# Performance work log

Hardware: AMD Instinct MI355X
Metric: run time of the kernel (lower is better)

Reference implementation:

```python
import jax, jax.numpy as jnp
import numpy as np

B, S, V = 2, 336, 8      # batch, seq_len, n_vars
D, H, P = 256, 8, 96     # d_model, num_heads, pred_len
DK = D // H
OUT_CHN = 8
EPS = 1e-5


def _layernorm(x, g, b):
    mu = jnp.mean(x, axis=-1, keepdims=True)
    var = jnp.var(x, axis=-1, keepdims=True)
    return (x - mu) * jax.lax.rsqrt(var + EPS) * g + b


def _attn_ff(src, Wq, bq, Wk, bk, Wv, bv, Wo, bo, ln1_g, ln1_b):
    # src: [N, L, D]; manual MHA + residual + layernorm (dropout=0)
    N, L, _ = src.shape
    q = (src @ Wq + bq).reshape(N, L, H, DK).transpose(0, 2, 1, 3)
    k = (src @ Wk + bk).reshape(N, L, H, DK).transpose(0, 2, 1, 3)
    v = (src @ Wv + bv).reshape(N, L, H, DK).transpose(0, 2, 1, 3)
    scores = jnp.einsum('nhqd,nhkd->nhqk', q, k) / np.sqrt(DK).astype(np.float32)
    attn = jax.nn.softmax(scores, axis=-1)
    o = jnp.einsum('nhqk,nhkd->nhqd', attn, v)
    o = o.transpose(0, 2, 1, 3).reshape(N, L, D) @ Wo + bo
    return _layernorm(src + o, ln1_g, ln1_b)


def setup_inputs() -> dict:
    key = jax.random.key(0)
    ks = jax.random.split(key, 8)
    s = 1.0 / np.sqrt(D)
    return {
        'x': jax.random.normal(ks[0], (B, S, V), dtype=jnp.float32),
        'emb_w': jax.random.normal(ks[1], (1, D), dtype=jnp.float32),
        'emb_b': jnp.zeros((D,), jnp.float32),
        'Wq': jax.random.normal(ks[2], (D, D), dtype=jnp.float32) * s,
        'bq': jnp.zeros((D,), jnp.float32),
        'Wk': jax.random.normal(ks[3], (D, D), dtype=jnp.float32) * s,
        'bk': jnp.zeros((D,), jnp.float32),
        'Wv': jax.random.normal(ks[4], (D, D), dtype=jnp.float32) * s,
        'bv': jnp.zeros((D,), jnp.float32),
        'Wo': jax.random.normal(ks[5], (D, D), dtype=jnp.float32) * s,
        'bo': jnp.zeros((D,), jnp.float32),
        'ln1_g': jnp.ones((D,), jnp.float32),
        'ln1_b': jnp.zeros((D,), jnp.float32),
        'norm_g': jnp.ones((D,), jnp.float32),
        'norm_b': jnp.zeros((D,), jnp.float32),
        'proj_w': jax.random.normal(ks[6], (S * D, P), dtype=jnp.float32) / np.sqrt(S * D).astype(np.float32),
        'proj_b': jnp.zeros((P,), jnp.float32),
    }


def reference(x, emb_w, emb_b, Wq, bq, Wk, bk, Wv, bv, Wo, bo,
              ln1_g, ln1_b, norm_g, norm_b, proj_w, proj_b):
    attn_p = (Wq, bq, Wk, bk, Wv, bv, Wo, bo, ln1_g, ln1_b)
    # x: [B,S,V] -> [B,V,S] -> embed each scalar to D
    e = x.transpose(0, 2, 1)[..., None] @ emb_w + emb_b  # [B,V,S,D]
    for _ in range(10):
        # attention over time axis (shared weights)
        e = _attn_ff(e.reshape(B * V, S, D), *attn_p).reshape(B, V, S, D)
        e = _layernorm(e.transpose(0, 2, 1, 3), norm_g, norm_b)  # [B,S,V,D]
        # attention over variable axis (same weights)
        e = _attn_ff(e.reshape(B * S, V, D), *attn_p).reshape(B, S, V, D)
        e = e.transpose(0, 2, 1, 3)  # [B,V,S,D]
    out = e.reshape(B, V, S * D) @ proj_w + proj_b  # [B,V,P]
    return out.transpose(0, 2, 1)[:, :, :OUT_CHN]  # [B,P,out_chn]
```

## Files before the change

### kernel.cpp

```cpp
#include <hip/hip_runtime.h>

#define SS 336
#define VV 8
#define DD 256
#define DKK 32
#define NTOK 5376
#define NTD (NTOK * DD)
#define ATT_SCALE 0.17677669529663687f
#define LN_EPS 1e-5f

typedef _Float16 f16x8 __attribute__((ext_vector_type(8)));
typedef _Float16 f16x4v __attribute__((ext_vector_type(4)));
typedef __attribute__((ext_vector_type(4))) float f32x4;

__device__ inline _Float16 f2h(float f) { return (_Float16)f; }

__global__ __launch_bounds__(256) void k_init(
    const float* __restrict__ Wq, const float* __restrict__ Wk,
    const float* __restrict__ Wv, const float* __restrict__ Wo,
    const float* __restrict__ x, const float* __restrict__ ew,
    const float* __restrict__ eb,
    _Float16* __restrict__ WT2, float* __restrict__ E,
    _Float16* __restrict__ E16, double* __restrict__ out64,
    int* __restrict__ cnt) {
  int bid = blockIdx.x;
  int tid = threadIdx.x;
  if (bid < 1024) {
    int z = bid >> 8;
    const float* W = (z == 0) ? Wq : (z == 1) ? Wk : (z == 2) ? Wv : Wo;
    int o = (bid & 255) * 256 + tid;
    int blk = o >> 9;
    int idx = o & 511;
    int lane = idx >> 3, j = idx & 7;
    int nt = blk >> 3, kb = blk & 7;
    int lcol = lane & 15, quad = lane >> 4;
    int n = nt * 16 + lcol;
    int k = kb * 32 + quad * 8 + j;
    WT2[(size_t)z * 65536 + o] = f2h(W[k * 256 + n]);
    if (bid == 0) {
      for (int i = tid; i < 1536; i += 256) atomicExch(&out64[i], 0.0);
      if (tid == 0) atomicExch(cnt, 0);
    }
  } else {
    int token = bid - 1024;
    int n = token / SS, s = token - n * SS;
    int b = n >> 3, v = n & 7;
    float xv = x[(b * SS + s) * VV + v];
    int d = tid;
    float val = fmaf(xv, ew[d], eb[d]);
    E[token * DD + d] = val;
    E16[token * DD + d] = f2h(val);
  }
}

#define KSTR 36
#define VTSTR 344
#define PSTR 72
#define QSTR 40
__global__ __launch_bounds__(512) void k_attn_time(
    const _Float16* __restrict__ Et16, const _Float16* __restrict__ Q16,
    const _Float16* __restrict__ K16, const _Float16* __restrict__ V16,
    const _Float16* __restrict__ WT2,
    const float* __restrict__ bq, const float* __restrict__ bk,
    const float* __restrict__ bv, _Float16* __restrict__ O16, int mode) {
  int qg = blockIdx.x, h = blockIdx.y, n = blockIdx.z;
  int tid = threadIdx.x;
  int wave = tid >> 6, lane = tid & 63;
  int quad = lane >> 4, lcol = lane & 15;

  __shared__ __align__(16) char SMRAW[143264];
  _Float16* Ks  = (_Float16*)SMRAW;
  _Float16* Vt  = (_Float16*)(SMRAW + 24192);
  _Float16* Qs  = (_Float16*)(SMRAW + 46240);
  _Float16* Wl  = (_Float16*)(SMRAW + 60320);
  _Float16* Ach = (_Float16*)(SMRAW + 109472);
  _Float16* PsB = (_Float16*)(mode ? SMRAW + 60320 : SMRAW + 46240);

  const size_t ebase = (size_t)(n * SS) * DD;
  const size_t base  = ebase + h * DKK;
  int qt0 = qg ? 11 : 0;
  int qtend = qg ? 21 : 11;

  const f32x4 z4 = {0.f, 0.f, 0.f, 0.f};

  if (mode) {
    {
      int h2 = h * 2;
      for (int c = tid; c < 3072; c += 512) {
        int ot = c >> 9, rest = c & 511;
        int z = (ot < 2) ? 1 : (ot < 4) ? 2 : 0;
        int nt = h2 + (ot & 1);
        *(f16x8*)&Wl[(ot << 12) + rest * 8] =
            *(const f16x8*)&WT2[(size_t)z * 65536 + nt * 4096 + rest * 8];
      }
      for (int c = tid; c < 272; c += 512) {
        if (c < 256) {
          int d = c >> 3, col = 336 + (c & 7);
          Vt[d * VTSTR + col] = (_Float16)0.f;
        } else {
          Vt[32 * VTSTR + (c - 256)] = (_Float16)0.f;
        }
      }
    }
    for (int ck = 0; ck < 6; ++ck) {
      int m0c = ck * 64;
      int nmt = (ck < 5) ? 4 : 1;
      __syncthreads();
      for (int c = tid; c < nmt * 16 * 32; c += 512) {
        int row = c >> 5, seg = c & 31;
        *(f16x8*)&Ach[row * 264 + seg * 8] =
            *(const f16x8*)&Et16[ebase + (size_t)(m0c + row) * 256 + seg * 8];
      }
      __syncthreads();
      int nU = nmt * 6;
      for (int u = wave; u < nU; u += 8) {
        int mtl = u / 6, ot = u % 6;
        int gt = ck * 4 + mtl;
        if (ot >= 4 && (gt < qt0 || gt >= qtend)) continue;
        f32x4 acc = z4;
#pragma unroll
        for (int kb = 0; kb < 8; ++kb) {
          f16x8 af = *(const f16x8*)&Ach[(mtl * 16 + lcol) * 264 + kb * 32 + quad * 8];
          f16x8 wf = *(const f16x8*)&Wl[(ot << 12) + kb * 512 + lane * 8];
          acc = __builtin_amdgcn_mfma_f32_16x16x32_f16(af, wf, acc, 0, 0, 0);
        }
        int dlo = ((ot & 1) << 4) + lcol;
        const float* bz = (ot < 2) ? bk : (ot < 4) ? bv : bq;
        float bval = bz[h * 32 + dlo];
        if (ot < 2) {
#pragma unroll
          for (int i = 0; i < 4; ++i)
            Ks[(m0c + mtl * 16 + quad * 4 + i) * KSTR + dlo] = f2h(acc[i] + bval);
        } else if (ot < 4) {
#pragma unroll
          for (int i = 0; i < 4; ++i)
            Vt[dlo * VTSTR + (m0c + mtl * 16 + quad * 4 + i)] = f2h(acc[i] + bval);
        } else {
          int ql = gt - qt0;
#pragma unroll
          for (int i = 0; i < 4; ++i)
            Qs[(ql * 16 + quad * 4 + i) * QSTR + dlo] = f2h(acc[i] + bval);
        }
      }
    }
    __syncthreads();
  } else {
    for (int c = tid; c < 1344; c += 512) {
      int row = c >> 2, part = c & 3;
      f16x8 kv = *(const f16x8*)&K16[base + (size_t)row * DD + part * 8];
      f16x4v klo = __builtin_shufflevector(kv, kv, 0, 1, 2, 3);
      f16x4v khi = __builtin_shufflevector(kv, kv, 4, 5, 6, 7);
      *(f16x4v*)&Ks[row * KSTR + part * 8] = klo;
      *(f16x4v*)&Ks[row * KSTR + part * 8 + 4] = khi;
      f16x8 vv = *(const f16x8*)&V16[base + (size_t)row * DD + part * 8];
#pragma unroll
      for (int j = 0; j < 8; ++j) Vt[(part * 8 + j) * VTSTR + row] = vv[j];
    }
    for (int c = tid; c < 272; c += 512) {
      if (c < 256) {
        int d = c >> 3, col = 336 + (c & 7);
        Vt[d * VTSTR + col] = (_Float16)0.f;
      } else {
        Vt[32 * VTSTR + (c - 256)] = (_Float16)0.f;
      }
    }
    __syncthreads();
  }

  _Float16* P = PsB + wave * (16 * PSTR);
  const f16x8 onesv = {(_Float16)1.f, (_Float16)1.f, (_Float16)1.f, (_Float16)1.f,
                       (_Float16)1.f, (_Float16)1.f, (_Float16)1.f, (_Float16)1.f};

  for (int qtile = qt0 + wave; qtile < qtend; qtile += 8) {
    int qb = qtile * 16;
    int ql = qtile - qt0;

    f16x8 qf;
    if (mode)
      qf = *(const f16x8*)&Qs[(ql * 16 + lcol) * QSTR + quad * 8];
    else
      qf = *(const f16x8*)&Q16[base + (size_t)(qb + lcol) * DD + quad * 8];
    f32x4 accA = {0.f, 0.f, 0.f, 0.f};
    f32x4 accB = {0.f, 0.f, 0.f, 0.f};
    f32x4 lacc = {0.f, 0.f, 0.f, 0.f};
    float m_[4] = {-1e30f, -1e30f, -1e30f, -1e30f};

    for (int T = 0; T < 6; ++T) {
      int k0 = T * 64;
      bool full = (T < 5);
      f32x4 s[4];
      {
        const _Float16* kp = &Ks[(k0 + lcol) * KSTR + quad * 8];
        f16x4v a0 = *(const f16x4v*)kp;
        f16x4v b0 = *(const f16x4v*)(kp + 4);
        f16x8 kf = __builtin_shufflevector(a0, b0, 0, 1, 2, 3, 4, 5, 6, 7);
        s[0] = __builtin_amdgcn_mfma_f32_16x16x32_f16(qf, kf, z4, 0, 0, 0);
      }
      if (full) {
#pragma unroll
        for (int u = 1; u < 4; ++u) {
          const _Float16* kp = &Ks[(k0 + u * 16 + lcol) * KSTR + quad * 8];
          f16x4v a0 = *(const f16x4v*)kp;
          f16x4v b0 = *(const f16x4v*)(kp + 4);
          f16x8 kf = __builtin_shufflevector(a0, b0, 0, 1, 2, 3, 4, 5, 6, 7);
          s[u] = __builtin_amdgcn_mfma_f32_16x16x32_f16(qf, kf, z4, 0, 0, 0);
        }
      } else {
        s[1] = z4; s[2] = z4; s[3] = z4;
      }
      float sc[4][4], p[4][4], corr[4];
#pragma unroll
      for (int u = 0; u < 4; ++u)
#pragma unroll
        for (int i = 0; i < 4; ++i)
          sc[u][i] = (u == 0 || full) ? s[u][i] * ATT_SCALE : -1e30f;
#pragma unroll
      for (int i = 0; i < 4; ++i) {
        float t2 = fmaxf(fmaxf(sc[0][i], sc[1][i]), fmaxf(sc[2][i], sc[3][i]));
        t2 = fmaxf(t2, __shfl_xor(t2, 1));
        t2 = fmaxf(t2, __shfl_xor(t2, 2));
        t2 = fmaxf(t2, __shfl_xor(t2, 4));
        t2 = fmaxf(t2, __shfl_xor(t2, 8));
        float nm = fmaxf(m_[i], t2);
        corr[i] = __expf(m_[i] - nm);
        m_[i] = nm;
#pragma unroll
        for (int u = 0; u < 4; ++u) p[u][i] = __expf(sc[u][i] - nm);
        accA[i] *= corr[i];
        accB[i] *= corr[i];
        lacc[i] *= corr[i];
      }
#pragma unroll
      for (int i = 0; i < 4; ++i)
#pragma unroll
        for (int u = 0; u < 4; ++u)
          P[(quad * 4 + i) * PSTR + u * 16 + lcol] = f2h(p[u][i]);
      f16x8 pf0 = *(const f16x8*)&P[lcol * PSTR + quad * 8];
      lacc = __builtin_amdgcn_mfma_f32_16x16x32_f16(pf0, onesv, lacc, 0, 0, 0);
      f16x8 va0 = *(const f16x8*)&Vt[lcol * VTSTR + k0 + quad * 8];
      f16x8 vb0 = *(const f16x8*)&Vt[(16 + lcol) * VTSTR + k0 + quad * 8];
      accA = __builtin_amdgcn_mfma_f32_16x16x32_f16(pf0, va0, accA, 0, 0, 0);
      accB = __builtin_amdgcn_mfma_f32_16x16x32_f16(pf0, vb0, accB, 0, 0, 0);
      if (full) {
        f16x8 pf1 = *(const f16x8*)&P[lcol * PSTR + 32 + quad * 8];
        lacc = __builtin_amdgcn_mfma_f32_16x16x32_f16(pf1, onesv, lacc, 0, 0, 0);
        f16x8 va1 = *(const f16x8*)&Vt[lcol * VTSTR + k0 + 32 + quad * 8];
        f16x8 vb1 = *(const f16x8*)&Vt[(16 + lcol) * VTSTR + k0 + 32 + quad * 8];
        accA = __builtin_amdgcn_mfma_f32_16x16x32_f16(pf1, va1, accA, 0, 0, 0);
        accB = __builtin_amdgcn_mfma_f32_16x16x32_f16(pf1, vb1, accB, 0, 0, 0);
      }
    }

#pragma unroll
    for (int i = 0; i < 4; ++i) {
      float inv = 1.f / lacc[i];
      P[(quad * 4 + i) * PSTR + lcol] = f2h(accA[i] * inv);
      P[(quad * 4 + i) * PSTR + 16 + lcol] = f2h(accB[i] * inv);
    }
    int row = lane >> 2, seg = lane & 3;
    f16x8 ov = *(const f16x8*)&P[row * PSTR + seg * 8];
    *(f16x8*)&O16[base + (size_t)(qb + row) * DD + seg * 8] = ov;
  }
}

__global__ __launch_bounds__(512) void k_mega_var(
    const _Float16* __restrict__ AO16, const _Float16* __restrict__ WT2,
    const float* __restrict__ bq, const float* __restrict__ bk,
    const float* __restrict__ bv, const float* __restrict__ bo,
    const float* __restrict__ g1, const float* __restrict__ c1,
    const float* __restrict__ gn, const float* __restrict__ bn,
    float* __restrict__ Etime, _Float16* __restrict__ Q16,
    _Float16* __restrict__ K16, _Float16* __restrict__ V16, int doqkv) {
  int tid = threadIdx.x;
  int wave = tid >> 6, lane = tid & 63;
  int quad = lane >> 4, lcol = lane & 15;

  __shared__ int rmapS[32];
  __shared__ _Float16 Af[32 * 264];
  __shared__ float Cf[32 * 260];
  __shared__ _Float16 QKVs[32 * 776];

  if (tid < 32) {
    int r2 = blockIdx.x * 32 + tid;
    int n_idx = r2 >> 3, v = r2 & 7;
    int b = n_idx / SS, s = n_idx - b * SS;
    rmapS[tid] = (b * VV + v) * SS + s;
  }
  __syncthreads();

  {
    int row = tid >> 4, seg = tid & 15;
    const _Float16* src = AO16 + (size_t)rmapS[row] * DD + seg * 16;
    _Float16* dst = Af + row * 264 + seg * 16;
    *(f16x8*)(dst) = *(const f16x8*)(src);
    *(f16x8*)(dst + 8) = *(const f16x8*)(src + 8);
  }
  __syncthreads();

  const _Float16* WoF = WT2 + (size_t)3 * 65536;

  {
    f32x4 acc[2][2] = {};
    for (int kb = 0; kb < 8; ++kb) {
      int k0 = kb * 32;
      f16x8 af0 = *(const f16x8*)&Af[lcol * 264 + k0 + quad * 8];
      f16x8 af1 = *(const f16x8*)&Af[(16 + lcol) * 264 + k0 + quad * 8];
#pragma unroll
      for (int nt = 0; nt < 2; ++nt) {
        f16x8 bfr = *(const f16x8*)&WoF[((wave * 2 + nt) * 8 + kb) * 512 + lane * 8];
        acc[0][nt] = __builtin_amdgcn_mfma_f32_16x16x32_f16(af0, bfr, acc[0][nt], 0, 0, 0);
        acc[1][nt] = __builtin_amdgcn_mfma_f32_16x16x32_f16(af1, bfr, acc[1][nt], 0, 0, 0);
      }
    }
#pragma unroll
    for (int mt = 0; mt < 2; ++mt) {
#pragma unroll
      for (int i = 0; i < 4; ++i) {
        int row = mt * 16 + quad * 4 + i;
        size_t rb = (size_t)rmapS[row] * 256;
#pragma unroll
        for (int nt = 0; nt < 2; ++nt) {
          int col = (wave * 2 + nt) * 16 + lcol;
          Cf[row * 260 + col] = acc[mt][nt][i] + bo[col] + Etime[rb + col];
        }
      }
    }
  }
  __syncthreads();

  {
    int row = tid >> 4, c0 = (tid & 15) * 16;
    float v[16];
#pragma unroll
    for (int j = 0; j < 16; ++j) v[j] = Cf[row * 260 + c0 + j];
#pragma unroll
    for (int pass = 0; pass < 2; ++pass) {
      const float* gg = pass ? gn : g1;
      const float* bb = pass ? bn : c1;
      float s = 0.f, q = 0.f;
#pragma unroll
      for (int j = 0; j < 16; ++j) { s += v[j]; q = fmaf(v[j], v[j], q); }
      s += __shfl_xor(s, 1); q += __shfl_xor(q, 1);
      s += __shfl_xor(s, 2); q += __shfl_xor(q, 2);
      s += __shfl_xor(s, 4); q += __shfl_xor(q, 4);
      s += __shfl_xor(s, 8); q += __shfl_xor(q, 8);
      float mu = s * (1.0f / 256.0f);
      float rs = rsqrtf(q * (1.0f / 256.0f) - mu * mu + LN_EPS);
#pragma unroll
      for (int j = 0; j < 16; ++j)
        v[j] = fmaf((v[j] - mu) * rs, gg[c0 + j], bb[c0 + j]);
    }
#pragma unroll
    for (int j = 0; j < 16; ++j) Cf[row * 260 + c0 + j] = v[j];
#pragma unroll
    for (int j8 = 0; j8 < 2; ++j8) {
      f16x8 h;
#pragma unroll
      for (int jj = 0; jj < 8; ++jj) h[jj] = f2h(v[j8 * 8 + jj]);
      *(f16x8*)&Af[row * 264 + c0 + j8 * 8] = h;
    }
  }
  __syncthreads();

  {
    f32x4 acc[2][6] = {};
    for (int kb = 0; kb < 8; ++kb) {
      int k0 = kb * 32;
      f16x8 af0 = *(const f16x8*)&Af[lcol * 264 + k0 + quad * 8];
      f16x8 af1 = *(const f16x8*)&Af[(16 + lcol) * 264 + k0 + quad * 8];
#pragma unroll
      for (int j = 0; j < 6; ++j) {
        int ntg = wave * 6 + j;
        f16x8 bfr = *(const f16x8*)&WT2[(size_t)(ntg * 8 + kb) * 512 + lane * 8];
        acc[0][j] = __builtin_amdgcn_mfma_f32_16x16x32_f16(af0, bfr, acc[0][j], 0, 0, 0);
        acc[1][j] = __builtin_amdgcn_mfma_f32_16x16x32_f16(af1, bfr, acc[1][j], 0, 0, 0);
      }
    }
#pragma unroll
    for (int j = 0; j < 6; ++j) {
      int ntg = wave * 6 + j;
      int colb = ntg * 16;
      int z = colb >> 8, coln = (colb & 255) + lcol;
      const float* bz = (z == 0) ? bq : (z == 1) ? bk : bv;
      float bval = bz[coln];
#pragma unroll
      for (int mt = 0; mt < 2; ++mt) {
#pragma unroll
        for (int i = 0; i < 4; ++i)
          QKVs[(mt * 16 + quad * 4 + i) * 776 + colb + lcol] = f2h(acc[mt][j][i] + bval);
      }
    }
  }
  __syncthreads();

  {
    int half = tid & 1, qi = (tid >> 1) & 7, h = (tid >> 4) & 7, ng = tid >> 7;
    int d0 = h * 32 + half * 16;
    const _Float16* Qp = &QKVs[(ng * 8 + qi) * 776 + d0];
    float qv[16];
#pragma unroll
    for (int j8 = 0; j8 < 2; ++j8) {
      f16x8 t = *(const f16x8*)(Qp + j8 * 8);
#pragma unroll
      for (int jj = 0; jj < 8; ++jj) qv[j8 * 8 + jj] = (float)t[jj];
    }
    float sc[8];
#pragma unroll
    for (int k = 0; k < 8; ++k) {
      const _Float16* Kp = &QKVs[(ng * 8 + k) * 776 + 256 + d0];
      float s = 0.f;
#pragma unroll
      for (int j8 = 0; j8 < 2; ++j8) {
        f16x8 t = *(const f16x8*)(Kp + j8 * 8);
#pragma unroll
        for (int jj = 0; jj < 8; ++jj) s = fmaf(qv[j8 * 8 + jj], (float)t[jj], s);
      }
      sc[k] = s;
    }
#pragma unroll
    for (int k = 0; k < 8; ++k)
      sc[k] = (sc[k] + __shfl_xor(sc[k], 1)) * ATT_SCALE;
    float mx = sc[0];
#pragma unroll
    for (int k = 1; k < 8; ++k) mx = fmaxf(mx, sc[k]);
    float ps = 0.f;
#pragma unroll
    for (int k = 0; k < 8; ++k) { sc[k] = __expf(sc[k] - mx); ps += sc[k]; }
    float inv = 1.f / ps;
    float ov[16];
#pragma unroll
    for (int j = 0; j < 16; ++j) ov[j] = 0.f;
#pragma unroll
    for (int k = 0; k < 8; ++k) {
      const _Float16* Vp = &QKVs[(ng * 8 + k) * 776 + 512 + d0];
      float p = sc[k];
#pragma unroll
      for (int j8 = 0; j8 < 2; ++j8) {
        f16x8 t = *(const f16x8*)(Vp + j8 * 8);
#pragma unroll
        for (int jj = 0; jj < 8; ++jj)
          ov[j8 * 8 + jj] = fmaf(p, (float)t[jj], ov[j8 * 8 + jj]);
      }
    }
    _Float16* Op = &Af[(ng * 8 + qi) * 264 + d0];
#pragma unroll
    for (int j8 = 0; j8 < 2; ++j8) {
      f16x8 hh;
#pragma unroll
      for (int jj = 0; jj < 8; ++jj) hh[jj] = f2h(ov[j8 * 8 + jj] * inv);
      *(f16x8*)(Op + j8 * 8) = hh;
    }
  }
  __syncthreads();

  {
    f32x4 acc[2][2] = {};
    for (int kb = 0; kb < 8; ++kb) {
      int k0 = kb * 32;
      f16x8 af0 = *(const f16x8*)&Af[lcol * 264 + k0 + quad * 8];
      f16x8 af1 = *(const f16x8*)&Af[(16 + lcol) * 264 + k0 + quad * 8];
#pragma unroll
      for (int nt = 0; nt < 2; ++nt) {
        f16x8 bfr = *(const f16x8*)&WoF[((wave * 2 + nt) * 8 + kb) * 512 + lane * 8];
        acc[0][nt] = __builtin_amdgcn_mfma_f32_16x16x32_f16(af0, bfr, acc[0][nt], 0, 0, 0);
        acc[1][nt] = __builtin_amdgcn_mfma_f32_16x16x32_f16(af1, bfr, acc[1][nt], 0, 0, 0);
      }
    }
#pragma unroll
    for (int mt = 0; mt < 2; ++mt) {
#pragma unroll
      for (int i = 0; i < 4; ++i) {
        int row = mt * 16 + quad * 4 + i;
#pragma unroll
        for (int nt = 0; nt < 2; ++nt) {
          int col = (wave * 2 + nt) * 16 + lcol;
          Cf[row * 260 + col] = acc[mt][nt][i] + bo[col] + Cf[row * 260 + col];
        }
      }
    }
  }
  __syncthreads();

  {
    int row = tid >> 4, c0 = (tid & 15) * 16;
    float v[16];
#pragma unroll
    for (int j = 0; j < 16; ++j) v[j] = Cf[row * 260 + c0 + j];
    float s = 0.f, q = 0.f;
#pragma unroll
    for (int j = 0; j < 16; ++j) { s += v[j]; q = fmaf(v[j], v[j], q); }
    s += __shfl_xor(s, 1); q += __shfl_xor(q, 1);
    s += __shfl_xor(s, 2); q += __shfl_xor(q, 2);
    s += __shfl_xor(s, 4); q += __shfl_xor(q, 4);
    s += __shfl_xor(s, 8); q += __shfl_xor(q, 8);
    float mu = s * (1.0f / 256.0f);
    float rs = rsqrtf(q * (1.0f / 256.0f) - mu * mu + LN_EPS);
#pragma unroll
    for (int j = 0; j < 16; ++j)
      v[j] = fmaf((v[j] - mu) * rs, g1[c0 + j], c1[c0 + j]);
    size_t rb = (size_t)rmapS[row] * 256 + c0;
#pragma unroll
    for (int j4 = 0; j4 < 4; ++j4) {
      float4 f4 = make_float4(v[j4 * 4], v[j4 * 4 + 1], v[j4 * 4 + 2], v[j4 * 4 + 3]);
      *(float4*)&Etime[rb + j4 * 4] = f4;
    }
#pragma unroll
    for (int j8 = 0; j8 < 2; ++j8) {
      f16x8 hh;
#pragma unroll
      for (int jj = 0; jj < 8; ++jj) hh[jj] = f2h(v[j8 * 8 + jj]);
      *(f16x8*)&Af[row * 264 + c0 + j8 * 8] = hh;
    }
  }
  __syncthreads();

  if (doqkv) {
    f32x4 acc[2][6] = {};
    for (int kb = 0; kb < 8; ++kb) {
      int k0 = kb * 32;
      f16x8 af0 = *(const f16x8*)&Af[lcol * 264 + k0 + quad * 8];
      f16x8 af1 = *(const f16x8*)&Af[(16 + lcol) * 264 + k0 + quad * 8];
#pragma unroll
      for (int j = 0; j < 6; ++j) {
        int ntg = wave * 6 + j;
        f16x8 bfr = *(const f16x8*)&WT2[(size_t)(ntg * 8 + kb) * 512 + lane * 8];
        acc[0][j] = __builtin_amdgcn_mfma_f32_16x16x32_f16(af0, bfr, acc[0][j], 0, 0, 0);
        acc[1][j] = __builtin_amdgcn_mfma_f32_16x16x32_f16(af1, bfr, acc[1][j], 0, 0, 0);
      }
    }
#pragma unroll
    for (int j = 0; j < 6; ++j) {
      int ntg = wave * 6 + j;
      int colb = ntg * 16;
      int z = colb >> 8, coln = (colb & 255) + lcol;
      const float* bz = (z == 0) ? bq : (z == 1) ? bk : bv;
      _Float16* Hd = (z == 0) ? Q16 : (z == 1) ? K16 : V16;
      float bval = bz[coln];
#pragma unroll
      for (int mt = 0; mt < 2; ++mt) {
#pragma unroll
        for (int i = 0; i < 4; ++i) {
          int row = mt * 16 + quad * 4 + i;
          Hd[(size_t)rmapS[row] * 256 + coln] = f2h(acc[mt][j][i] + bval);
        }
      }
    }
  }
}

__global__ __launch_bounds__(192) void k_proj(
    const float* __restrict__ E, const float* __restrict__ PW,
    const float* __restrict__ PB, double* __restrict__ out64,
    int* __restrict__ cnt, float* __restrict__ out) {
  int kc = blockIdx.x;
  int tid = threadIdx.x;
  int p4 = tid % 24, g = tid / 24;
  __shared__ float Es[16][128];
  __shared__ float sm[8][1536];
  __shared__ int win;
  for (int idx = tid; idx < 512; idx += 192) {
    int row = idx >> 5, kk4 = idx & 31;
    *(float4*)&Es[row][kk4 * 4] =
        *(const float4*)&E[(size_t)row * 86016 + kc * 128 + kk4 * 4];
  }
  __syncthreads();
  float4 acc[16];
#pragma unroll
  for (int i = 0; i < 16; ++i) acc[i] = make_float4(0.f, 0.f, 0.f, 0.f);
  for (int j = 0; j < 16; ++j) {
    int k = g * 16 + j;
    float4 w = *(const float4*)&PW[(size_t)(kc * 128 + k) * 96 + p4 * 4];
#pragma unroll
    for (int row = 0; row < 16; ++row) {
      float e = Es[row][k];
      acc[row].x = fmaf(e, w.x, acc[row].x);
      acc[row].y = fmaf(e, w.y, acc[row].y);
      acc[row].z = fmaf(e, w.z, acc[row].z);
      acc[row].w = fmaf(e, w.w, acc[row].w);
    }
  }
#pragma unroll
  for (int row = 0; row < 16; ++row)
    *(float4*)&sm[g][row * 96 + p4 * 4] = acc[row];
  __syncthreads();
  for (int o = tid; o < 1536; o += 192) {
    float s = 0.f;
#pragma unroll
    for (int g2 = 0; g2 < 8; ++g2) s += sm[g2][o];
    atomicAdd(&out64[o], (double)s);
  }
  __threadfence();
  __syncthreads();
  if (tid == 0) {
    int old = atomicAdd(cnt, 1);
    win = (old == 671) ? 1 : 0;
  }
  __syncthreads();
  if (win) {
    __threadfence();
    for (int j = tid; j < 1536; j += 192) {
      double t = atomicAdd(&out64[j], 0.0);
      int row = j / 96, p = j - row * 96;
      int b = row >> 3, v = row & 7;
      out[b * 768 + p * 8 + v] = PB[p] + (float)t;
    }
  }
}

extern "C" void kernel_launch(void* const* d_in, const int* in_sizes, int n_in,
                              void* d_out, int out_size, void* d_ws,
                              size_t ws_size, hipStream_t stream) {
  const float* x     = (const float*)d_in[0];
  const float* emb_w = (const float*)d_in[1];
  const float* emb_b = (const float*)d_in[2];
  const float* Wq = (const float*)d_in[3];
  const float* bq = (const float*)d_in[4];
  const float* Wk = (const float*)d_in[5];
  const float* bk = (const float*)d_in[6];
  const float* Wv = (const float*)d_in[7];
  const float* bv = (const float*)d_in[8];
  const float* Wo = (const float*)d_in[9];
  const float* bo = (const float*)d_in[10];
  const float* g1 = (const float*)d_in[11];
  const float* b1 = (const float*)d_in[12];
  const float* gn = (const float*)d_in[13];
  const float* bn = (const float*)d_in[14];
  const float* PW = (const float*)d_in[15];
  const float* PB = (const float*)d_in[16];
  float* out = (float*)d_out;

  float* ws = (float*)d_ws;
  float* Etime   = ws;
  _Float16* Et16 = (_Float16*)(ws + (size_t)NTD);
  _Float16* Q16  = (_Float16*)(ws + (size_t)NTD + NTD / 2);
  _Float16* K16  = Q16 + (size_t)NTD;
  _Float16* V16  = K16 + (size_t)NTD;
  _Float16* AO16 = V16 + (size_t)NTD;
  _Float16* WT2  = AO16 + (size_t)NTD;
  double* out64  = (double*)(WT2 + 4 * 65536);
  int* cnt       = (int*)(out64 + 1536);

  k_init<<<6400, 256, 0, stream>>>(Wq, Wk, Wv, Wo, x, emb_w, emb_b,
                                   WT2, Etime, Et16, out64, cnt);
  for (int it = 0; it < 10; ++it) {
    k_attn_time<<<dim3(2, 8, 16), 512, 0, stream>>>(
        Et16, Q16, K16, V16, WT2, bq, bk, bv, AO16, (it == 0) ? 1 : 0);
    k_mega_var<<<168, 512, 0, stream>>>(
        AO16, WT2, bq, bk, bv, bo, g1, b1, gn, bn, Etime,
        Q16, K16, V16, (it < 9) ? 1 : 0);
  }
  k_proj<<<672, 192, 0, stream>>>(Etime, PW, PB, out64, cnt, out);
}
```

Baseline: 588.2 us.

## Simplify final projection to direct float atomics with bias pre-initialized

The final projection kernel now splits K into 256 chunks of 336 and has each thread accumulate one row of four outputs, adding the partial sums straight into the output with float atomics. This replaces the double-precision scratch buffer, the block-level reduction in shared memory and the last-block-finishes counter. The bias is written into the output during the init kernel. The change removes the counter/fence handshake and the shared-memory reduction, at the cost of more global float atomics and a summation order that is no longer deterministic.

```diff
diff --git a/kernel.cpp b/kernel.cpp
--- a/kernel.cpp
+++ b/kernel.cpp
@@ -19,10 +19,9 @@
     const float* __restrict__ Wq, const float* __restrict__ Wk,
     const float* __restrict__ Wv, const float* __restrict__ Wo,
     const float* __restrict__ x, const float* __restrict__ ew,
-    const float* __restrict__ eb,
+    const float* __restrict__ eb, const float* __restrict__ PB,
     _Float16* __restrict__ WT2, float* __restrict__ E,
-    _Float16* __restrict__ E16, double* __restrict__ out64,
-    int* __restrict__ cnt) {
+    _Float16* __restrict__ E16, float* __restrict__ out) {
   int bid = blockIdx.x;
   int tid = threadIdx.x;
   if (bid < 1024) {
@@ -38,8 +37,10 @@
     int k = kb * 32 + quad * 8 + j;
     WT2[(size_t)z * 65536 + o] = f2h(W[k * 256 + n]);
     if (bid == 0) {
-      for (int i = tid; i < 1536; i += 256) atomicExch(&out64[i], 0.0);
-      if (tid == 0) atomicExch(cnt, 0);
+      for (int i = tid; i < 1536; i += 256) {
+        int row = i / 96, p = i - row * 96;
+        out[(row >> 3) * 768 + p * 8 + (row & 7)] = PB[p];
+      }
     }
   } else {
     int token = bid - 1024;
@@ -548,63 +549,36 @@
   }
 }
 
-__global__ __launch_bounds__(192) void k_proj(
+__global__ __launch_bounds__(384) void k_proj(
     const float* __restrict__ E, const float* __restrict__ PW,
-    const float* __restrict__ PB, double* __restrict__ out64,
-    int* __restrict__ cnt, float* __restrict__ out) {
-  int kc = blockIdx.x;
+    float* __restrict__ out) {
+  __shared__ float Es[16][336];
   int tid = threadIdx.x;
-  int p4 = tid % 24, g = tid / 24;
-  __shared__ float Es[16][128];
-  __shared__ float sm[8][1536];
-  __shared__ int win;
-  for (int idx = tid; idx < 512; idx += 192) {
-    int row = idx >> 5, kk4 = idx & 31;
+  int kc0 = blockIdx.x * 336;
+  for (int idx = tid; idx < 1344; idx += 384) {
+    int row = idx / 84, kk4 = idx % 84;
     *(float4*)&Es[row][kk4 * 4] =
-        *(const float4*)&E[(size_t)row * 86016 + kc * 128 + kk4 * 4];
-  }
-  __syncthreads();
-  float4 acc[16];
-#pragma unroll
-  for (int i = 0; i < 16; ++i) acc[i] = make_float4(0.f, 0.f, 0.f, 0.f);
-  for (int j = 0; j < 16; ++j) {
-    int k = g * 16 + j;
-    float4 w = *(const float4*)&PW[(size_t)(kc * 128 + k) * 96 + p4 * 4];
-#pragma unroll
-    for (int row = 0; row < 16; ++row) {
-      float e = Es[row][k];
-      acc[row].x = fmaf(e, w.x, acc[row].x);
-      acc[row].y = fmaf(e, w.y, acc[row].y);
-      acc[row].z = fmaf(e, w.z, acc[row].z);
-      acc[row].w = fmaf(e, w.w, acc[row].w);
-    }
-  }
-#pragma unroll
-  for (int row = 0; row < 16; ++row)
-    *(float4*)&sm[g][row * 96 + p4 * 4] = acc[row];
-  __syncthreads();
-  for (int o = tid; o < 1536; o += 192) {
-    float s = 0.f;
-#pragma unroll
-    for (int g2 = 0; g2 < 8; ++g2) s += sm[g2][o];
-    atomicAdd(&out64[o], (double)s);
-  }
-  __threadfence();
-  __syncthreads();
-  if (tid == 0) {
-    int old = atomicAdd(cnt, 1);
-    win = (old == 671) ? 1 : 0;
-  }
-  __syncthreads();
-  if (win) {
-    __threadfence();
-    for (int j = tid; j < 1536; j += 192) {
-      double t = atomicAdd(&out64[j], 0.0);
-      int row = j / 96, p = j - row * 96;
-      int b = row >> 3, v = row & 7;
-      out[b * 768 + p * 8 + v] = PB[p] + (float)t;
-    }
-  }
+        *(const float4*)&E[(size_t)row * 86016 + kc0 + kk4 * 4];
+  }
+  __syncthreads();
+  int r = tid / 24, p4 = tid % 24;
+  const float* ErP = Es[r];
+  float4 acc = make_float4(0.f, 0.f, 0.f, 0.f);
+#pragma unroll 4
+  for (int k = 0; k < 336; ++k) {
+    float e = ErP[k];
+    float4 w = *(const float4*)&PW[(size_t)(kc0 + k) * 96 + p4 * 4];
+    acc.x = fmaf(e, w.x, acc.x);
+    acc.y = fmaf(e, w.y, acc.y);
+    acc.z = fmaf(e, w.z, acc.z);
+    acc.w = fmaf(e, w.w, acc.w);
+  }
+  int b = r >> 3, v = r & 7;
+  float* o = &out[b * 768 + v];
+  atomicAdd(&o[(p4 * 4 + 0) * 8], acc.x);
+  atomicAdd(&o[(p4 * 4 + 1) * 8], acc.y);
+  atomicAdd(&o[(p4 * 4 + 2) * 8], acc.z);
+  atomicAdd(&o[(p4 * 4 + 3) * 8], acc.w);
 }
 
 extern "C" void kernel_launch(void* const* d_in, const int* in_sizes, int n_in,
@@ -637,11 +611,9 @@
   _Float16* V16  = K16 + (size_t)NTD;
   _Float16* AO16 = V16 + (size_t)NTD;
   _Float16* WT2  = AO16 + (size_t)NTD;
-  double* out64  = (double*)(WT2 + 4 * 65536);
-  int* cnt       = (int*)(out64 + 1536);
-
-  k_init<<<6400, 256, 0, stream>>>(Wq, Wk, Wv, Wo, x, emb_w, emb_b,
-                                   WT2, Etime, Et16, out64, cnt);
+
+  k_init<<<6400, 256, 0, stream>>>(Wq, Wk, Wv, Wo, x, emb_w, emb_b, PB,
+                                   WT2, Etime, Et16, out);
   for (int it = 0; it < 10; ++it) {
     k_attn_time<<<dim3(2, 8, 16), 512, 0, stream>>>(
         Et16, Q16, K16, V16, WT2, bq, bk, bv, AO16, (it == 0) ? 1 : 0);
@@ -649,5 +621,5 @@
         AO16, WT2, bq, bk, bv, bo, g1, b1, gn, bn, Etime,
         Q16, K16, V16, (it < 9) ? 1 : 0);
   }
-  k_proj<<<672, 192, 0, stream>>>(Etime, PW, PB, out64, cnt, out);
+  k_proj<<<256, 384, 0, stream>>>(Etime, PW, out);
 }
```

Result: slower. 603.5 us (+2.6%).
